# Kernel optimization log

Measured on AMD Instinct MI355X. Metric: run time of the kernel, lower is better.

The kernel has to match this reference:

```python
import jax, jax.numpy as jnp
import numpy as np

SEQ = 4096
R_DIM = 1024
Z_DIM = 1024
AT_DIM = 1024
G_DIM = 1024


def _xavier(key, shape):
    fan_in, fan_out = shape[1], shape[0]
    limit = float(np.sqrt(6.0 / (fan_in + fan_out)))
    return jax.random.uniform(key, shape, jnp.float32, -limit, limit)


def setup_inputs() -> dict:
    key = jax.random.key(0)
    ks = jax.random.split(key, 12)
    return {
        "R": jax.random.normal(ks[0], (SEQ, R_DIM), jnp.float32),
        "W_alpha": _xavier(ks[1], (R_DIM, 2 * R_DIM)),
        "b_alpha": jnp.zeros((R_DIM,), jnp.float32),
        "W_delta": _xavier(ks[2], (R_DIM, 2 * R_DIM)),
        "b_delta": jnp.zeros((R_DIM,), jnp.float32),
        "W_q": _xavier(ks[3], (AT_DIM, Z_DIM)),
        "b_q": jnp.zeros((AT_DIM,), jnp.float32),
        "W_k": _xavier(ks[4], (AT_DIM, Z_DIM)),
        "b_k": jnp.zeros((AT_DIM,), jnp.float32),
        "W_v": _xavier(ks[5], (AT_DIM, Z_DIM)),
        "b_v": jnp.zeros((AT_DIM,), jnp.float32),
        "W_z": _xavier(ks[6], (Z_DIM, R_DIM)),
        "b_z": jnp.zeros((Z_DIM,), jnp.float32),
        "W_f": _xavier(ks[7], (AT_DIM, G_DIM)),
        "b_f": jnp.zeros((AT_DIM,), jnp.float32),
        "W_EMA": _xavier(ks[8], (G_DIM, R_DIM)),
        "b_EMA": jnp.zeros((G_DIM,), jnp.float32),
        "W_z_at": _xavier(ks[9], (G_DIM, AT_DIM)),
        "b_z_at": jnp.zeros((G_DIM,), jnp.float32),
        "W_i": _xavier(ks[10], (1, R_DIM)),
        "b_i": jnp.zeros((1,), jnp.float32),
        "W_final": _xavier(ks[11], (1, G_DIM)),
    }


def reference(R, W_alpha, b_alpha, W_delta, b_delta, W_q, b_q, W_k, b_k,
              W_v, b_v, W_z, b_z, W_f, b_f, W_EMA, b_EMA, W_z_at, b_z_at,
              W_i, b_i, W_final):
    r_dim = R.shape[-1]
    at_dim = W_q.shape[0]
    # prepend zero row; r_t / r_{t-1} pairs
    R2 = jnp.concatenate([jnp.zeros((1, r_dim), R.dtype), R], axis=0)
    r_t, r_prev = R2[1:], R2[:-1]
    concat_r = jnp.concatenate([r_prev, r_t], axis=1)  # [m, 2r]
    alpha = jnp.tanh(concat_r @ W_alpha.T + b_alpha)
    delta = jnp.tanh(concat_r @ W_delta.T + b_delta)
    R_EMA = alpha * r_t + (1.0 - alpha) * delta * r_prev
    Z = jax.nn.silu(R_EMA @ W_z.T + b_z)
    Q = Z @ W_q.T + b_q
    K = Z @ W_k.T + b_k
    V = Z @ W_v.T + b_v
    scores = (Q @ K.T) / jnp.sqrt(jnp.float32(at_dim))  # [m, m]
    weights = jax.nn.softmax(scores, axis=-1)
    Z_at = weights @ V
    R_EMA_p = R_EMA @ W_EMA.T + b_EMA
    f = jax.nn.sigmoid(R_EMA_p @ W_f.T + b_f)
    Z_at_p = f * Z_at
    Z_EMA_f = Z_at_p @ W_z_at.T + b_z_at
    Z_tp = jnp.tanh(R_EMA_p + Z_EMA_f)
    i = jnp.tanh(R_EMA @ W_i.T + b_i)  # [m, 1]
    Z_final = i * Z_tp + (1.0 - i) * R_EMA_p
    p_hat = jax.nn.sigmoid(Z_final @ W_final.T)  # [m, 1]
    return p_hat
```

## Files before the change

kernel.cpp:

```cpp
#include <hip/hip_runtime.h>
#include <cstdint>
#include <cmath>

#define MB (1024ull * 1024ull)

typedef unsigned short u16;
typedef __attribute__((ext_vector_type(8))) short short8;
typedef __attribute__((ext_vector_type(4))) float f32x4;

enum { M_TANH = 0, M_ZRE = 1, M_QKVF = 2, M_SCALE = 3, M_PVRAW = 4, M_F32 = 5 };

__device__ __forceinline__ u16 f2b(float f) {
  union { float f; uint32_t u; } v; v.f = f;
  uint32_t r = v.u + 0x7FFFu + ((v.u >> 16) & 1u);
  return (u16)(r >> 16);
}
__device__ __forceinline__ float b2f(u16 u) {
  union { uint32_t u; float f; } v; v.u = ((uint32_t)u) << 16;
  return v.f;
}

typedef __attribute__((address_space(3))) uint32_t lds_u32;
typedef const __attribute__((address_space(1))) uint32_t glb_u32;

__device__ __forceinline__ void gload16(const void* g, void* l) {
  __builtin_amdgcn_global_load_lds((glb_u32*)g, (lds_u32*)l, 16, 0, 0);
}

template <int MODE>
__global__ __launch_bounds__(256) void gemm(const u16* __restrict__ A,
                                            const u16* __restrict__ B,
                                            const float* __restrict__ bias,
                                            const u16* __restrict__ A2,
                                            const u16* __restrict__ B2,
                                            const float* __restrict__ bias2,
                                            u16* __restrict__ Cb,
                                            u16* __restrict__ Cb2,
                                            u16* __restrict__ Cb3,
                                            float* __restrict__ Cf,
                                            int K, int lda, int ldb, float scale) {
  constexpr int NI = 4;
  constexpr int NJ = 2;
  __shared__ u16 As[3][64 * 32];
  __shared__ u16 Bs[3][128 * 32];
  const int tid = threadIdx.x;
  const int wid = tid >> 6, lane = tid & 63;

  const int gx = gridDim.x, nwg = gx * gridDim.y;
  int id = blockIdx.y * gx + blockIdx.x;
  if ((nwg & 7) == 0) id = (id & 7) * (nwg >> 3) + (id >> 3);
  const int bm = (id / gx) * 64, bn = (id % gx) * 128;
  const int colbase = wid * 32;

  const bool isf = (MODE == M_QKVF) && (bn >= 3072);
  const u16* Ab = isf ? A2 : A;
  const u16* Bb = isf ? B2 : B;
  const int bnl = isf ? bn - 3072 : bn;
  const int kofs = (MODE == M_PVRAW) ? (int)blockIdx.z * K : 0;

  const int srow = tid >> 2;
  const int schunk = (tid & 3) ^ ((srow >> 1) & 3);
  const u16* gA = Ab + (size_t)(bm + srow) * lda + kofs + schunk * 8;
  const u16* gB = Bb + (size_t)(bnl + srow) * ldb + kofs + schunk * 8;

  f32x4 acc[NI][NJ];
#pragma unroll
  for (int i = 0; i < NI; ++i)
#pragma unroll
    for (int j = 0; j < NJ; ++j) acc[i][j] = (f32x4){0.f, 0.f, 0.f, 0.f};

  const int ar = lane & 15;
  const int pch = (((lane >> 4) ^ ((ar >> 1) & 3))) * 8;

  const int NT = K >> 5;

  auto stage = [&](int buf, int t) {
    const u16* a = gA + (size_t)t * 32;
    const u16* b = gB + (size_t)t * 32;
    gload16(a, &As[buf][wid * 512]);
    gload16(b, &Bs[buf][wid * 512]);
    gload16(b + (size_t)64 * ldb, &Bs[buf][wid * 512 + 2048]);
  };

  stage(0, 0);
  stage(1, 1);
  int cb = 0;
  for (int t = 0; t < NT; ++t) {
    if (t + 1 < NT) asm volatile("s_waitcnt vmcnt(3)" ::: "memory");
    else            asm volatile("s_waitcnt vmcnt(0)" ::: "memory");
    __builtin_amdgcn_s_barrier();
    if (t + 2 < NT) stage((cb + 2) % 3, t + 2);
    short8 af[NI], bf[NJ];
#pragma unroll
    for (int i = 0; i < NI; ++i)
      af[i] = *reinterpret_cast<const short8*>(&As[cb][(i * 16 + ar) * 32 + pch]);
#pragma unroll
    for (int j = 0; j < NJ; ++j)
      bf[j] = *reinterpret_cast<const short8*>(&Bs[cb][(colbase + j * 16 + ar) * 32 + pch]);
    __builtin_amdgcn_s_setprio(1);
#pragma unroll
    for (int i = 0; i < NI; ++i)
#pragma unroll
      for (int j = 0; j < NJ; ++j)
        acc[i][j] = __builtin_amdgcn_mfma_f32_16x16x32_bf16(af[i], bf[j], acc[i][j], 0, 0, 0);
    __builtin_amdgcn_s_setprio(0);
    cb = (cb == 2) ? 0 : cb + 1;
  }

  float* Cfz = Cf;
  if (MODE == M_PVRAW && blockIdx.z != 0) Cfz = (float*)Cb3;

#pragma unroll
  for (int i = 0; i < NI; ++i) {
    const int rb = bm + i * 16 + (lane >> 4) * 4;
#pragma unroll
    for (int j = 0; j < NJ; ++j) {
      const int n = bn + colbase + j * 16 + (lane & 15);
#pragma unroll
      for (int r = 0; r < 4; ++r) {
        const int m = rb + r;
        float v = acc[i][j][r];
        if (MODE == M_TANH) {
          v = tanhf(v + bias[n]);
          Cb[(size_t)m * 2048 + n] = f2b(v);
        } else if (MODE == M_ZRE) {
          v += bias[n];
          if (n < 1024) { const float s = v / (1.f + expf(-v)); Cb[(size_t)m * 1024 + n] = f2b(s); }
          else Cb2[(size_t)m * 1024 + (n - 1024)] = f2b(v);
        } else if (MODE == M_QKVF) {
          if (isf) {
            const int nl = n - 3072;
            const float s = 1.f / (1.f + expf(-(v + bias2[nl])));
            Cb3[(size_t)m * 1024 + nl] = f2b(s);
          } else {
            v += bias[n];
            if (n < 2048) Cb[(size_t)m * 2048 + n] = f2b(v);
            else Cb2[(size_t)m * 1024 + (n - 2048)] = f2b(v);
          }
        } else if (MODE == M_SCALE) {
          Cb[(size_t)m * 4096 + n] = f2b(v * scale);
        } else if (MODE == M_PVRAW) {
          Cfz[(size_t)m * 1024 + n] = v;
        } else if (MODE == M_F32) {
          Cf[(size_t)m * 1024 + n] = v + bias[n];
        }
      }
    }
  }
}

__global__ __launch_bounds__(256) void pv_reduce(const float* __restrict__ p0,
                                                 const float* __restrict__ p1,
                                                 const u16* __restrict__ fvb,
                                                 u16* __restrict__ Zatp) {
  const int idx = blockIdx.x * 256 + threadIdx.x;
  const float4 a = reinterpret_cast<const float4*>(p0)[idx];
  const float4 b = reinterpret_cast<const float4*>(p1)[idx];
  const ushort4 f4 = reinterpret_cast<const ushort4*>(fvb)[idx];
  ushort4 o;
  o.x = f2b((a.x + b.x) * b2f(f4.x));
  o.y = f2b((a.y + b.y) * b2f(f4.y));
  o.z = f2b((a.z + b.z) * b2f(f4.z));
  o.w = f2b((a.w + b.w) * b2f(f4.w));
  reinterpret_cast<ushort4*>(Zatp)[idx] = o;
}

__global__ __launch_bounds__(256) void convert_all(
    const float* __restrict__ s0, const float* __restrict__ s1, const float* __restrict__ s2,
    const float* __restrict__ s3, const float* __restrict__ s4, const float* __restrict__ s5,
    const float* __restrict__ s6, const float* __restrict__ s7, const float* __restrict__ s8,
    u16* __restrict__ Wad, u16* __restrict__ Wze, u16* __restrict__ Wqkv,
    u16* __restrict__ Wfb, u16* __restrict__ Wzab) {
  const int idx = blockIdx.x * 256 + threadIdx.x;
  const float* src; u16* dst; int off;
  if      (idx < 524288)  { src = s0; dst = Wad;           off = idx; }
  else if (idx < 1048576) { src = s1; dst = Wad + 2097152; off = idx - 524288; }
  else if (idx < 1310720) { src = s2; dst = Wze;           off = idx - 1048576; }
  else if (idx < 1572864) { src = s3; dst = Wze + 1048576; off = idx - 1310720; }
  else if (idx < 1835008) { src = s4; dst = Wqkv;          off = idx - 1572864; }
  else if (idx < 2097152) { src = s5; dst = Wqkv + 1048576; off = idx - 1835008; }
  else if (idx < 2359296) { src = s6; dst = Wqkv + 2097152; off = idx - 2097152; }
  else if (idx < 2621440) { src = s7; dst = Wfb;           off = idx - 2359296; }
  else                    { src = s8; dst = Wzab;          off = idx - 2621440; }
  const float4 v = reinterpret_cast<const float4*>(src)[off];
  ushort4 o; o.x = f2b(v.x); o.y = f2b(v.y); o.z = f2b(v.z); o.w = f2b(v.w);
  reinterpret_cast<ushort4*>(dst)[off] = o;
}

__global__ void copy_bias(const float* __restrict__ ba, const float* __restrict__ bd,
                          const float* __restrict__ bz, const float* __restrict__ be,
                          const float* __restrict__ bq, const float* __restrict__ bk,
                          const float* __restrict__ bv,
                          float* __restrict__ bad, float* __restrict__ bze,
                          float* __restrict__ bqkv) {
  const int t = threadIdx.x;
  const float4* src; float4* dst;
  switch (blockIdx.x) {
    case 0: src = (const float4*)ba; dst = (float4*)bad; break;
    case 1: src = (const float4*)bd; dst = (float4*)(bad + 1024); break;
    case 2: src = (const float4*)bz; dst = (float4*)bze; break;
    case 3: src = (const float4*)be; dst = (float4*)(bze + 1024); break;
    case 4: src = (const float4*)bq; dst = (float4*)bqkv; break;
    case 5: src = (const float4*)bk; dst = (float4*)(bqkv + 1024); break;
    default: src = (const float4*)bv; dst = (float4*)(bqkv + 2048); break;
  }
  dst[t] = src[t];
}

__global__ __launch_bounds__(256) void concat_kern(const float* __restrict__ R,
                                                   u16* __restrict__ Rc) {
  const int idx = blockIdx.x * 256 + threadIdx.x;
  const int m = idx >> 9;
  const int c = (idx & 511) * 4;
  float4 v;
  if (c < 1024) {
    if (m > 0) v = *reinterpret_cast<const float4*>(&R[(size_t)(m - 1) * 1024 + c]);
    else v = make_float4(0.f, 0.f, 0.f, 0.f);
  } else {
    v = *reinterpret_cast<const float4*>(&R[(size_t)m * 1024 + (c - 1024)]);
  }
  ushort4 o; o.x = f2b(v.x); o.y = f2b(v.y); o.z = f2b(v.z); o.w = f2b(v.w);
  reinterpret_cast<ushort4*>(Rc)[idx] = o;
}

__global__ __launch_bounds__(256) void ema_combine(const float* __restrict__ R,
                                                   const u16* __restrict__ adb,
                                                   u16* __restrict__ REMA) {
  const int idx = blockIdx.x * 256 + threadIdx.x;
  const int m = idx >> 8, c4 = idx & 255;
  const float4 rt = reinterpret_cast<const float4*>(R)[idx];
  float4 rp = make_float4(0.f, 0.f, 0.f, 0.f);
  if (m > 0) rp = reinterpret_cast<const float4*>(R)[idx - 256];
  const ushort4 a4 = reinterpret_cast<const ushort4*>(adb)[m * 512 + c4];
  const ushort4 d4 = reinterpret_cast<const ushort4*>(adb)[m * 512 + 256 + c4];
  ushort4 o;
  { const float av = b2f(a4.x); o.x = f2b(av * rt.x + (1.f - av) * b2f(d4.x) * rp.x); }
  { const float av = b2f(a4.y); o.y = f2b(av * rt.y + (1.f - av) * b2f(d4.y) * rp.y); }
  { const float av = b2f(a4.z); o.z = f2b(av * rt.z + (1.f - av) * b2f(d4.z) * rp.z); }
  { const float av = b2f(a4.w); o.w = f2b(av * rt.w + (1.f - av) * b2f(d4.w) * rp.w); }
  reinterpret_cast<ushort4*>(REMA)[idx] = o;
}

__device__ __forceinline__ float waveMax(float v) {
#pragma unroll
  for (int o = 32; o; o >>= 1) v = fmaxf(v, __shfl_down(v, o));
  return v;
}
__device__ __forceinline__ float waveSum(float v) {
#pragma unroll
  for (int o = 32; o; o >>= 1) v += __shfl_down(v, o);
  return v;
}

__global__ __launch_bounds__(256) void softmax_rows(u16* __restrict__ S) {
  u16* p = S + (size_t)blockIdx.x * 4096;
  const int tid = threadIdx.x;
  float v[16];
#pragma unroll
  for (int j = 0; j < 4; ++j) {
    const ushort4 t = *reinterpret_cast<const ushort4*>(&p[tid * 4 + 1024 * j]);
    v[4 * j + 0] = b2f(t.x); v[4 * j + 1] = b2f(t.y);
    v[4 * j + 2] = b2f(t.z); v[4 * j + 3] = b2f(t.w);
  }
  float mx = -INFINITY;
#pragma unroll
  for (int j = 0; j < 16; ++j) mx = fmaxf(mx, v[j]);
  __shared__ float red[4];
  const float wm = waveMax(mx);
  if ((tid & 63) == 0) red[tid >> 6] = wm;
  __syncthreads();
  mx = fmaxf(fmaxf(red[0], red[1]), fmaxf(red[2], red[3]));
  __syncthreads();
  float sum = 0.f;
#pragma unroll
  for (int j = 0; j < 16; ++j) { v[j] = expf(v[j] - mx); sum += v[j]; }
  const float ws_ = waveSum(sum);
  if ((tid & 63) == 0) red[tid >> 6] = ws_;
  __syncthreads();
  const float inv = 1.f / (red[0] + red[1] + red[2] + red[3]);
#pragma unroll
  for (int j = 0; j < 4; ++j) {
    ushort4 t;
    t.x = f2b(v[4 * j + 0] * inv); t.y = f2b(v[4 * j + 1] * inv);
    t.z = f2b(v[4 * j + 2] * inv); t.w = f2b(v[4 * j + 3] * inv);
    *reinterpret_cast<ushort4*>(&p[tid * 4 + 1024 * j]) = t;
  }
}

__global__ __launch_bounds__(256) void transpose_b16(const u16* __restrict__ V,
                                                     u16* __restrict__ Vt) {
  __shared__ u16 t[64][72];
  const int bn = blockIdx.x * 64;
  const int bk = blockIdx.y * 64;
  const int tx = threadIdx.x & 15, ty = threadIdx.x >> 4;
#pragma unroll
  for (int i = 0; i < 64; i += 16) {
    const ushort4 v = *reinterpret_cast<const ushort4*>(&V[(size_t)(bk + ty + i) * 1024 + bn + tx * 4]);
    t[ty + i][tx * 4 + 0] = v.x; t[ty + i][tx * 4 + 1] = v.y;
    t[ty + i][tx * 4 + 2] = v.z; t[ty + i][tx * 4 + 3] = v.w;
  }
  __syncthreads();
#pragma unroll
  for (int i = 0; i < 64; i += 16) {
    ushort4 w;
    w.x = t[tx * 4 + 0][ty + i]; w.y = t[tx * 4 + 1][ty + i];
    w.z = t[tx * 4 + 2][ty + i]; w.w = t[tx * 4 + 3][ty + i];
    *reinterpret_cast<ushort4*>(&Vt[(size_t)(bn + ty + i) * 4096 + bk + tx * 4]) = w;
  }
}

__global__ void final_kern(const u16* __restrict__ REMAb, const u16* __restrict__ REMApb,
                           const float* __restrict__ ZEMAf,
                           const float* __restrict__ Wi, const float* __restrict__ bi,
                           const float* __restrict__ Wfin, float* __restrict__ out) {
  const int m = blockIdx.x, l = threadIdx.x;
  float si = 0.f;
#pragma unroll
  for (int j = 0; j < 16; ++j) {
    const int n = l + 64 * j;
    si += b2f(REMAb[(size_t)m * 1024 + n]) * Wi[n];
  }
#pragma unroll
  for (int o = 32; o; o >>= 1) si += __shfl_xor(si, o);
  const float im = tanhf(si + bi[0]);
  float s = 0.f;
#pragma unroll
  for (int j = 0; j < 16; ++j) {
    const int n = l + 64 * j;
    const float rp = b2f(REMApb[(size_t)m * 1024 + n]);
    const float zf = im * tanhf(rp + ZEMAf[(size_t)m * 1024 + n]) + (1.f - im) * rp;
    s += zf * Wfin[n];
  }
#pragma unroll
  for (int o = 32; o; o >>= 1) s += __shfl_down(s, o);
  if (l == 0) out[m] = 1.f / (1.f + expf(-s));
}

extern "C" void kernel_launch(void* const* d_in, const int* in_sizes, int n_in,
                              void* d_out, int out_size, void* d_ws, size_t ws_size,
                              hipStream_t stream) {
  const float* R       = (const float*)d_in[0];
  const float* W_alpha = (const float*)d_in[1];  const float* b_alpha = (const float*)d_in[2];
  const float* W_delta = (const float*)d_in[3];  const float* b_delta = (const float*)d_in[4];
  const float* W_q     = (const float*)d_in[5];  const float* b_q     = (const float*)d_in[6];
  const float* W_k     = (const float*)d_in[7];  const float* b_k     = (const float*)d_in[8];
  const float* W_v     = (const float*)d_in[9];  const float* b_v     = (const float*)d_in[10];
  const float* W_z     = (const float*)d_in[11]; const float* b_z     = (const float*)d_in[12];
  const float* W_f     = (const float*)d_in[13]; const float* b_f     = (const float*)d_in[14];
  const float* W_EMA   = (const float*)d_in[15]; const float* b_EMA   = (const float*)d_in[16];
  const float* W_z_at  = (const float*)d_in[17]; const float* b_z_at  = (const float*)d_in[18];
  const float* W_i     = (const float*)d_in[19]; const float* b_i     = (const float*)d_in[20];
  const float* W_final = (const float*)d_in[21];
  float* out = (float*)d_out;
  uint8_t* w8 = (uint8_t*)d_ws;

  u16*   Rc     = (u16*)(w8 + 0 * MB);
  u16*   Zb     = (u16*)(w8 + 0 * MB);
  u16*   Zatpb  = (u16*)(w8 + 0 * MB);
  u16*   REMApb = (u16*)(w8 + 8 * MB);
  u16*   Wad    = (u16*)(w8 + 16 * MB);
  u16*   fvb    = (u16*)(w8 + 16 * MB);
  u16*   adb    = (u16*)(w8 + 24 * MB);
  float* pvp0   = (float*)(w8 + 24 * MB);
  float* ZEMAf  = (float*)(w8 + 24 * MB);
  u16*   Wqkv   = (u16*)(w8 + 40 * MB);
  u16*   Vtb    = (u16*)(w8 + 40 * MB);
  u16*   Wze    = (u16*)(w8 + 46 * MB);
  u16*   Wfb    = (u16*)(w8 + 50 * MB);
  u16*   Wzab   = (u16*)(w8 + 52 * MB);
  u16*   REMAb  = (u16*)(w8 + 54 * MB);
  u16*   QKb    = (u16*)(w8 + 62 * MB);
  float* pvp1   = (float*)(w8 + 62 * MB);
  u16*   Vb     = (u16*)(w8 + 78 * MB);
  u16*   Sb     = (u16*)(w8 + 78 * MB);
  float* bad    = (float*)(w8 + 110 * MB + 64 * 1024);
  float* bze    = bad + 2048;
  float* bqkv   = bze + 2048;

  const dim3 blk(256);
  convert_all<<<11264, blk, 0, stream>>>(W_alpha, W_delta, W_z, W_EMA, W_q, W_k, W_v, W_f, W_z_at,
                                         Wad, Wze, Wqkv, Wfb, Wzab);
  concat_kern<<<8192, blk, 0, stream>>>(R, Rc);
  copy_bias<<<7, blk, 0, stream>>>(b_alpha, b_delta, b_z, b_EMA, b_q, b_k, b_v, bad, bze, bqkv);

  gemm<M_TANH><<<dim3(16, 64), blk, 0, stream>>>(
      Rc, Wad, bad, nullptr, nullptr, nullptr, adb, nullptr, nullptr, nullptr, 2048, 2048, 2048, 1.f);
  ema_combine<<<4096, blk, 0, stream>>>(R, adb, REMAb);
  gemm<M_ZRE><<<dim3(16, 64), blk, 0, stream>>>(
      REMAb, Wze, bze, nullptr, nullptr, nullptr, Zb, REMApb, nullptr, nullptr, 1024, 1024, 1024, 1.f);
  gemm<M_QKVF><<<dim3(32, 64), blk, 0, stream>>>(
      Zb, Wqkv, bqkv, REMApb, Wfb, b_f, QKb, Vb, fvb, nullptr, 1024, 1024, 1024, 1.f);
  transpose_b16<<<dim3(16, 64), blk, 0, stream>>>(Vb, Vtb);
  gemm<M_SCALE><<<dim3(32, 64), blk, 0, stream>>>(
      QKb, QKb + 1024, nullptr, nullptr, nullptr, nullptr, Sb, nullptr, nullptr, nullptr, 1024, 2048, 2048, 0.03125f);
  softmax_rows<<<4096, blk, 0, stream>>>(Sb);
  gemm<M_PVRAW><<<dim3(8, 64, 2), blk, 0, stream>>>(
      Sb, Vtb, nullptr, nullptr, nullptr, nullptr, nullptr, nullptr, (u16*)pvp1, pvp0, 2048, 4096, 4096, 1.f);
  pv_reduce<<<4096, blk, 0, stream>>>(pvp0, pvp1, fvb, Zatpb);
  gemm<M_F32><<<dim3(8, 64), blk, 0, stream>>>(
      Zatpb, Wzab, b_z_at, nullptr, nullptr, nullptr, nullptr, nullptr, nullptr, ZEMAf, 1024, 1024, 1024, 1.f);
  final_kern<<<4096, 64, 0, stream>>>(REMAb, REMApb, ZEMAf, W_i, b_i, W_final, out);
}
```

Before: 351.6 us.

## Fuse EMA combine into GEMM epilogue, drop PV split-K, use fast math

Interleaves the alpha and delta weight rows so each lane pair holds alpha and delta for the same column, letting the first GEMM epilogue compute R_EMA directly and removing the ema_combine kernel and its intermediate buffer. The concat kernel is merged into the weight conversion launch. The PV GEMM drops split-K and the reduce kernel, applying the f gate in its epilogue instead. The GEMM pipeline also moves from a triple-buffered async-wait scheme to double buffering with __syncthreads, and tanh/sigmoid/exp switch to __expf-based approximations. The risks are less overlap in the main loop and fewer workgroups (512) in the PV GEMM.

```diff
diff --git a/kernel.cpp b/kernel.cpp
--- a/kernel.cpp
+++ b/kernel.cpp
@@ -8,7 +8,7 @@
 typedef __attribute__((ext_vector_type(8))) short short8;
 typedef __attribute__((ext_vector_type(4))) float f32x4;
 
-enum { M_TANH = 0, M_ZRE = 1, M_QKVF = 2, M_SCALE = 3, M_PVRAW = 4, M_F32 = 5 };
+enum { M_EMA = 0, M_ZRE = 1, M_QKVF = 2, M_SCALE = 3, M_PVMUL = 4, M_F32 = 5 };
 
 __device__ __forceinline__ u16 f2b(float f) {
   union { float f; uint32_t u; } v; v.f = f;
@@ -18,6 +18,12 @@
 __device__ __forceinline__ float b2f(u16 u) {
   union { uint32_t u; float f; } v; v.u = ((uint32_t)u) << 16;
   return v.f;
+}
+__device__ __forceinline__ float tanh_fast(float x) {
+  return 1.f - 2.f / (1.f + __expf(2.f * x));
+}
+__device__ __forceinline__ float sigmoid_fast(float x) {
+  return 1.f / (1.f + __expf(-x));
 }
 
 typedef __attribute__((address_space(3))) uint32_t lds_u32;
@@ -34,15 +40,17 @@
                                             const u16* __restrict__ A2,
                                             const u16* __restrict__ B2,
                                             const float* __restrict__ bias2,
+                                            const u16* __restrict__ auxb,
                                             u16* __restrict__ Cb,
                                             u16* __restrict__ Cb2,
                                             u16* __restrict__ Cb3,
                                             float* __restrict__ Cf,
+                                            const float* __restrict__ R,
                                             int K, int lda, int ldb, float scale) {
   constexpr int NI = 4;
   constexpr int NJ = 2;
-  __shared__ u16 As[3][64 * 32];
-  __shared__ u16 Bs[3][128 * 32];
+  __shared__ u16 As[2][64 * 32];
+  __shared__ u16 Bs[2][128 * 32];
   const int tid = threadIdx.x;
   const int wid = tid >> 6, lane = tid & 63;
 
@@ -56,12 +64,11 @@
   const u16* Ab = isf ? A2 : A;
   const u16* Bb = isf ? B2 : B;
   const int bnl = isf ? bn - 3072 : bn;
-  const int kofs = (MODE == M_PVRAW) ? (int)blockIdx.z * K : 0;
 
   const int srow = tid >> 2;
   const int schunk = (tid & 3) ^ ((srow >> 1) & 3);
-  const u16* gA = Ab + (size_t)(bm + srow) * lda + kofs + schunk * 8;
-  const u16* gB = Bb + (size_t)(bnl + srow) * ldb + kofs + schunk * 8;
+  const u16* gA = Ab + (size_t)(bm + srow) * lda + schunk * 8;
+  const u16* gB = Bb + (size_t)(bnl + srow) * ldb + schunk * 8;
 
   f32x4 acc[NI][NJ];
 #pragma unroll
@@ -83,20 +90,17 @@
   };
 
   stage(0, 0);
-  stage(1, 1);
-  int cb = 0;
+  __syncthreads();
+  int cur = 0;
   for (int t = 0; t < NT; ++t) {
-    if (t + 1 < NT) asm volatile("s_waitcnt vmcnt(3)" ::: "memory");
-    else            asm volatile("s_waitcnt vmcnt(0)" ::: "memory");
-    __builtin_amdgcn_s_barrier();
-    if (t + 2 < NT) stage((cb + 2) % 3, t + 2);
+    if (t + 1 < NT) stage(cur ^ 1, t + 1);
     short8 af[NI], bf[NJ];
 #pragma unroll
     for (int i = 0; i < NI; ++i)
-      af[i] = *reinterpret_cast<const short8*>(&As[cb][(i * 16 + ar) * 32 + pch]);
+      af[i] = *reinterpret_cast<const short8*>(&As[cur][(i * 16 + ar) * 32 + pch]);
 #pragma unroll
     for (int j = 0; j < NJ; ++j)
-      bf[j] = *reinterpret_cast<const short8*>(&Bs[cb][(colbase + j * 16 + ar) * 32 + pch]);
+      bf[j] = *reinterpret_cast<const short8*>(&Bs[cur][(colbase + j * 16 + ar) * 32 + pch]);
     __builtin_amdgcn_s_setprio(1);
 #pragma unroll
     for (int i = 0; i < NI; ++i)
@@ -104,34 +108,38 @@
       for (int j = 0; j < NJ; ++j)
         acc[i][j] = __builtin_amdgcn_mfma_f32_16x16x32_bf16(af[i], bf[j], acc[i][j], 0, 0, 0);
     __builtin_amdgcn_s_setprio(0);
-    cb = (cb == 2) ? 0 : cb + 1;
-  }
-
-  float* Cfz = Cf;
-  if (MODE == M_PVRAW && blockIdx.z != 0) Cfz = (float*)Cb3;
+    __syncthreads();
+    cur ^= 1;
+  }
 
 #pragma unroll
   for (int i = 0; i < NI; ++i) {
     const int rb = bm + i * 16 + (lane >> 4) * 4;
 #pragma unroll
     for (int j = 0; j < NJ; ++j) {
-      const int n = bn + colbase + j * 16 + (lane & 15);
+      const int n = bn + colbase + j * 16 + ar;
 #pragma unroll
       for (int r = 0; r < 4; ++r) {
         const int m = rb + r;
         float v = acc[i][j][r];
-        if (MODE == M_TANH) {
-          v = tanhf(v + bias[n]);
-          Cb[(size_t)m * 2048 + n] = f2b(v);
+        if (MODE == M_EMA) {
+          v = tanh_fast(v + bias[n]);
+          const float vp = __shfl_xor(v, 1);
+          if ((lane & 1) == 0) {
+            const int jc = n >> 1;
+            const float rt = R[(size_t)m * 1024 + jc];
+            const float rp = (m > 0) ? R[(size_t)(m - 1) * 1024 + jc] : 0.f;
+            const float rema = v * rt + (1.f - v) * vp * rp;
+            Cb[(size_t)m * 1024 + jc] = f2b(rema);
+          }
         } else if (MODE == M_ZRE) {
           v += bias[n];
-          if (n < 1024) { const float s = v / (1.f + expf(-v)); Cb[(size_t)m * 1024 + n] = f2b(s); }
+          if (n < 1024) Cb[(size_t)m * 1024 + n] = f2b(v * sigmoid_fast(v));
           else Cb2[(size_t)m * 1024 + (n - 1024)] = f2b(v);
         } else if (MODE == M_QKVF) {
           if (isf) {
             const int nl = n - 3072;
-            const float s = 1.f / (1.f + expf(-(v + bias2[nl])));
-            Cb3[(size_t)m * 1024 + nl] = f2b(s);
+            Cb3[(size_t)m * 1024 + nl] = f2b(sigmoid_fast(v + bias2[nl]));
           } else {
             v += bias[n];
             if (n < 2048) Cb[(size_t)m * 2048 + n] = f2b(v);
@@ -139,8 +147,9 @@
           }
         } else if (MODE == M_SCALE) {
           Cb[(size_t)m * 4096 + n] = f2b(v * scale);
-        } else if (MODE == M_PVRAW) {
-          Cfz[(size_t)m * 1024 + n] = v;
+        } else if (MODE == M_PVMUL) {
+          v *= b2f(auxb[(size_t)m * 1024 + n]);
+          Cb[(size_t)m * 1024 + n] = f2b(v);
         } else if (MODE == M_F32) {
           Cf[(size_t)m * 1024 + n] = v + bias[n];
         }
@@ -149,42 +158,48 @@
   }
 }
 
-__global__ __launch_bounds__(256) void pv_reduce(const float* __restrict__ p0,
-                                                 const float* __restrict__ p1,
-                                                 const u16* __restrict__ fvb,
-                                                 u16* __restrict__ Zatp) {
-  const int idx = blockIdx.x * 256 + threadIdx.x;
-  const float4 a = reinterpret_cast<const float4*>(p0)[idx];
-  const float4 b = reinterpret_cast<const float4*>(p1)[idx];
-  const ushort4 f4 = reinterpret_cast<const ushort4*>(fvb)[idx];
-  ushort4 o;
-  o.x = f2b((a.x + b.x) * b2f(f4.x));
-  o.y = f2b((a.y + b.y) * b2f(f4.y));
-  o.z = f2b((a.z + b.z) * b2f(f4.z));
-  o.w = f2b((a.w + b.w) * b2f(f4.w));
-  reinterpret_cast<ushort4*>(Zatp)[idx] = o;
-}
-
 __global__ __launch_bounds__(256) void convert_all(
     const float* __restrict__ s0, const float* __restrict__ s1, const float* __restrict__ s2,
     const float* __restrict__ s3, const float* __restrict__ s4, const float* __restrict__ s5,
     const float* __restrict__ s6, const float* __restrict__ s7, const float* __restrict__ s8,
+    const float* __restrict__ R,
     u16* __restrict__ Wad, u16* __restrict__ Wze, u16* __restrict__ Wqkv,
-    u16* __restrict__ Wfb, u16* __restrict__ Wzab) {
+    u16* __restrict__ Wfb, u16* __restrict__ Wzab, u16* __restrict__ Rc) {
   const int idx = blockIdx.x * 256 + threadIdx.x;
-  const float* src; u16* dst; int off;
-  if      (idx < 524288)  { src = s0; dst = Wad;           off = idx; }
-  else if (idx < 1048576) { src = s1; dst = Wad + 2097152; off = idx - 524288; }
-  else if (idx < 1310720) { src = s2; dst = Wze;           off = idx - 1048576; }
-  else if (idx < 1572864) { src = s3; dst = Wze + 1048576; off = idx - 1310720; }
-  else if (idx < 1835008) { src = s4; dst = Wqkv;          off = idx - 1572864; }
+  if (idx >= 2883584) {
+    const int off = idx - 2883584;
+    const int m = off >> 9;
+    const int c = (off & 511) * 4;
+    float4 v;
+    if (c < 1024) {
+      if (m > 0) v = *reinterpret_cast<const float4*>(&R[(size_t)(m - 1) * 1024 + c]);
+      else v = make_float4(0.f, 0.f, 0.f, 0.f);
+    } else {
+      v = *reinterpret_cast<const float4*>(&R[(size_t)m * 1024 + (c - 1024)]);
+    }
+    ushort4 o; o.x = f2b(v.x); o.y = f2b(v.y); o.z = f2b(v.z); o.w = f2b(v.w);
+    reinterpret_cast<ushort4*>(Rc)[off] = o;
+    return;
+  }
+  const float* src; u16* dst; int off; int dstoff = -1;
+  if (idx < 524288) {
+    src = s0; dst = Wad; off = idx;
+    dstoff = ((off >> 9) * 2) * 512 + (off & 511);
+  } else if (idx < 1048576) {
+    src = s1; dst = Wad; off = idx - 524288;
+    dstoff = ((off >> 9) * 2 + 1) * 512 + (off & 511);
+  }
+  else if (idx < 1310720) { src = s2; dst = Wze;            off = idx - 1048576; }
+  else if (idx < 1572864) { src = s3; dst = Wze + 1048576;  off = idx - 1310720; }
+  else if (idx < 1835008) { src = s4; dst = Wqkv;           off = idx - 1572864; }
   else if (idx < 2097152) { src = s5; dst = Wqkv + 1048576; off = idx - 1835008; }
   else if (idx < 2359296) { src = s6; dst = Wqkv + 2097152; off = idx - 2097152; }
-  else if (idx < 2621440) { src = s7; dst = Wfb;           off = idx - 2359296; }
-  else                    { src = s8; dst = Wzab;          off = idx - 2621440; }
+  else if (idx < 2621440) { src = s7; dst = Wfb;            off = idx - 2359296; }
+  else                    { src = s8; dst = Wzab;           off = idx - 2621440; }
+  if (dstoff < 0) dstoff = off;
   const float4 v = reinterpret_cast<const float4*>(src)[off];
   ushort4 o; o.x = f2b(v.x); o.y = f2b(v.y); o.z = f2b(v.z); o.w = f2b(v.w);
-  reinterpret_cast<ushort4*>(dst)[off] = o;
+  reinterpret_cast<ushort4*>(dst)[dstoff] = o;
 }
 
 __global__ void copy_bias(const float* __restrict__ ba, const float* __restrict__ bd,
@@ -194,10 +209,18 @@
                           float* __restrict__ bad, float* __restrict__ bze,
                           float* __restrict__ bqkv) {
   const int t = threadIdx.x;
+  if (blockIdx.x == 0) {
+#pragma unroll
+    for (int k = 0; k < 4; ++k) bad[2 * (t + 256 * k)] = ba[t + 256 * k];
+    return;
+  }
+  if (blockIdx.x == 1) {
+#pragma unroll
+    for (int k = 0; k < 4; ++k) bad[2 * (t + 256 * k) + 1] = bd[t + 256 * k];
+    return;
+  }
   const float4* src; float4* dst;
   switch (blockIdx.x) {
-    case 0: src = (const float4*)ba; dst = (float4*)bad; break;
-    case 1: src = (const float4*)bd; dst = (float4*)(bad + 1024); break;
     case 2: src = (const float4*)bz; dst = (float4*)bze; break;
     case 3: src = (const float4*)be; dst = (float4*)(bze + 1024); break;
     case 4: src = (const float4*)bq; dst = (float4*)bqkv; break;
@@ -207,40 +230,6 @@
   dst[t] = src[t];
 }
 
-__global__ __launch_bounds__(256) void concat_kern(const float* __restrict__ R,
-                                                   u16* __restrict__ Rc) {
-  const int idx = blockIdx.x * 256 + threadIdx.x;
-  const int m = idx >> 9;
-  const int c = (idx & 511) * 4;
-  float4 v;
-  if (c < 1024) {
-    if (m > 0) v = *reinterpret_cast<const float4*>(&R[(size_t)(m - 1) * 1024 + c]);
-    else v = make_float4(0.f, 0.f, 0.f, 0.f);
-  } else {
-    v = *reinterpret_cast<const float4*>(&R[(size_t)m * 1024 + (c - 1024)]);
-  }
-  ushort4 o; o.x = f2b(v.x); o.y = f2b(v.y); o.z = f2b(v.z); o.w = f2b(v.w);
-  reinterpret_cast<ushort4*>(Rc)[idx] = o;
-}
-
-__global__ __launch_bounds__(256) void ema_combine(const float* __restrict__ R,
-                                                   const u16* __restrict__ adb,
-                                                   u16* __restrict__ REMA) {
-  const int idx = blockIdx.x * 256 + threadIdx.x;
-  const int m = idx >> 8, c4 = idx & 255;
-  const float4 rt = reinterpret_cast<const float4*>(R)[idx];
-  float4 rp = make_float4(0.f, 0.f, 0.f, 0.f);
-  if (m > 0) rp = reinterpret_cast<const float4*>(R)[idx - 256];
-  const ushort4 a4 = reinterpret_cast<const ushort4*>(adb)[m * 512 + c4];
-  const ushort4 d4 = reinterpret_cast<const ushort4*>(adb)[m * 512 + 256 + c4];
-  ushort4 o;
-  { const float av = b2f(a4.x); o.x = f2b(av * rt.x + (1.f - av) * b2f(d4.x) * rp.x); }
-  { const float av = b2f(a4.y); o.y = f2b(av * rt.y + (1.f - av) * b2f(d4.y) * rp.y); }
-  { const float av = b2f(a4.z); o.z = f2b(av * rt.z + (1.f - av) * b2f(d4.z) * rp.z); }
-  { const float av = b2f(a4.w); o.w = f2b(av * rt.w + (1.f - av) * b2f(d4.w) * rp.w); }
-  reinterpret_cast<ushort4*>(REMA)[idx] = o;
-}
-
 __device__ __forceinline__ float waveMax(float v) {
 #pragma unroll
   for (int o = 32; o; o >>= 1) v = fmaxf(v, __shfl_down(v, o));
@@ -273,7 +262,7 @@
   __syncthreads();
   float sum = 0.f;
 #pragma unroll
-  for (int j = 0; j < 16; ++j) { v[j] = expf(v[j] - mx); sum += v[j]; }
+  for (int j = 0; j < 16; ++j) { v[j] = __expf(v[j] - mx); sum += v[j]; }
   const float ws_ = waveSum(sum);
   if ((tid & 63) == 0) red[tid >> 6] = ws_;
   __syncthreads();
@@ -322,18 +311,18 @@
   }
 #pragma unroll
   for (int o = 32; o; o >>= 1) si += __shfl_xor(si, o);
-  const float im = tanhf(si + bi[0]);
+  const float im = tanh_fast(si + bi[0]);
   float s = 0.f;
 #pragma unroll
   for (int j = 0; j < 16; ++j) {
     const int n = l + 64 * j;
     const float rp = b2f(REMApb[(size_t)m * 1024 + n]);
-    const float zf = im * tanhf(rp + ZEMAf[(size_t)m * 1024 + n]) + (1.f - im) * rp;
+    const float zf = im * tanh_fast(rp + ZEMAf[(size_t)m * 1024 + n]) + (1.f - im) * rp;
     s += zf * Wfin[n];
   }
 #pragma unroll
   for (int o = 32; o; o >>= 1) s += __shfl_down(s, o);
-  if (l == 0) out[m] = 1.f / (1.f + expf(-s));
+  if (l == 0) out[m] = sigmoid_fast(s);
 }
 
 extern "C" void kernel_launch(void* const* d_in, const int* in_sizes, int n_in,
@@ -360,8 +349,6 @@
   u16*   REMApb = (u16*)(w8 + 8 * MB);
   u16*   Wad    = (u16*)(w8 + 16 * MB);
   u16*   fvb    = (u16*)(w8 + 16 * MB);
-  u16*   adb    = (u16*)(w8 + 24 * MB);
-  float* pvp0   = (float*)(w8 + 24 * MB);
   float* ZEMAf  = (float*)(w8 + 24 * MB);
   u16*   Wqkv   = (u16*)(w8 + 40 * MB);
   u16*   Vtb    = (u16*)(w8 + 40 * MB);
@@ -370,7 +357,6 @@
   u16*   Wzab   = (u16*)(w8 + 52 * MB);
   u16*   REMAb  = (u16*)(w8 + 54 * MB);
   u16*   QKb    = (u16*)(w8 + 62 * MB);
-  float* pvp1   = (float*)(w8 + 62 * MB);
   u16*   Vb     = (u16*)(w8 + 78 * MB);
   u16*   Sb     = (u16*)(w8 + 78 * MB);
   float* bad    = (float*)(w8 + 110 * MB + 64 * 1024);
@@ -378,26 +364,23 @@
   float* bqkv   = bze + 2048;
 
   const dim3 blk(256);
-  convert_all<<<11264, blk, 0, stream>>>(W_alpha, W_delta, W_z, W_EMA, W_q, W_k, W_v, W_f, W_z_at,
-                                         Wad, Wze, Wqkv, Wfb, Wzab);
-  concat_kern<<<8192, blk, 0, stream>>>(R, Rc);
+  convert_all<<<19456, blk, 0, stream>>>(W_alpha, W_delta, W_z, W_EMA, W_q, W_k, W_v, W_f, W_z_at,
+                                         R, Wad, Wze, Wqkv, Wfb, Wzab, Rc);
   copy_bias<<<7, blk, 0, stream>>>(b_alpha, b_delta, b_z, b_EMA, b_q, b_k, b_v, bad, bze, bqkv);
 
-  gemm<M_TANH><<<dim3(16, 64), blk, 0, stream>>>(
-      Rc, Wad, bad, nullptr, nullptr, nullptr, adb, nullptr, nullptr, nullptr, 2048, 2048, 2048, 1.f);
-  ema_combine<<<4096, blk, 0, stream>>>(R, adb, REMAb);
+  gemm<M_EMA><<<dim3(16, 64), blk, 0, stream>>>(
+      Rc, Wad, bad, nullptr, nullptr, nullptr, nullptr, REMAb, nullptr, nullptr, nullptr, R, 2048, 2048, 2048, 1.f);
   gemm<M_ZRE><<<dim3(16, 64), blk, 0, stream>>>(
-      REMAb, Wze, bze, nullptr, nullptr, nullptr, Zb, REMApb, nullptr, nullptr, 1024, 1024, 1024, 1.f);
+      REMAb, Wze, bze, nullptr, nullptr, nullptr, nullptr, Zb, REMApb, nullptr, nullptr, nullptr, 1024, 1024, 1024, 1.f);
   gemm<M_QKVF><<<dim3(32, 64), blk, 0, stream>>>(
-      Zb, Wqkv, bqkv, REMApb, Wfb, b_f, QKb, Vb, fvb, nullptr, 1024, 1024, 1024, 1.f);
+      Zb, Wqkv, bqkv, REMApb, Wfb, b_f, nullptr, QKb, Vb, fvb, nullptr, nullptr, 1024, 1024, 1024, 1.f);
   transpose_b16<<<dim3(16, 64), blk, 0, stream>>>(Vb, Vtb);
   gemm<M_SCALE><<<dim3(32, 64), blk, 0, stream>>>(
-      QKb, QKb + 1024, nullptr, nullptr, nullptr, nullptr, Sb, nullptr, nullptr, nullptr, 1024, 2048, 2048, 0.03125f);
+      QKb, QKb + 1024, nullptr, nullptr, nullptr, nullptr, nullptr, Sb, nullptr, nullptr, nullptr, nullptr, 1024, 2048, 2048, 0.03125f);
   softmax_rows<<<4096, blk, 0, stream>>>(Sb);
-  gemm<M_PVRAW><<<dim3(8, 64, 2), blk, 0, stream>>>(
-      Sb, Vtb, nullptr, nullptr, nullptr, nullptr, nullptr, nullptr, (u16*)pvp1, pvp0, 2048, 4096, 4096, 1.f);
-  pv_reduce<<<4096, blk, 0, stream>>>(pvp0, pvp1, fvb, Zatpb);
+  gemm<M_PVMUL><<<dim3(8, 64), blk, 0, stream>>>(
+      Sb, Vtb, nullptr, nullptr, nullptr, nullptr, fvb, Zatpb, nullptr, nullptr, nullptr, nullptr, 4096, 4096, 4096, 1.f);
   gemm<M_F32><<<dim3(8, 64), blk, 0, stream>>>(
-      Zatpb, Wzab, b_z_at, nullptr, nullptr, nullptr, nullptr, nullptr, nullptr, ZEMAf, 1024, 1024, 1024, 1.f);
+      Zatpb, Wzab, b_z_at, nullptr, nullptr, nullptr, nullptr, nullptr, nullptr, nullptr, ZEMAf, nullptr, 1024, 1024, 1024, 1.f);
   final_kern<<<4096, 64, 0, stream>>>(REMAb, REMApb, ZEMAf, W_i, b_i, W_final, out);
 }
```

Result: faster. 338.6 us (-3.7%).
